# Kernel optimization log

Measured on AMD Instinct MI355X. Metric: run time of the kernel, lower is better.

Reference implementation:

```python
import jax, jax.numpy as jnp
import numpy as np

N = 128000      # total nodes
B = 128         # graphs, 1000 nodes each
L = 4           # max_levels
S_MAX = 1000    # max cluster size (<= PositionalEncoding max_len)
H = 128         # hidden dim (all conv output dims equal)
IN_DIM = 128
OUT_DIM = 1
E = 1024000
TEMP = 0.1


def layer_norm(x, g, b, eps=1e-5):
    mu = jnp.mean(x, axis=-1, keepdims=True)
    v = jnp.mean((x - mu) ** 2, axis=-1, keepdims=True)
    return (x - mu) * jax.lax.rsqrt(v + eps) * g + b


def transformer_conv(x, src, dst, Wq, bq, Wk, bk, Wv, bv, Ws, bs):
    # PyG TransformerConv, heads=1: softmax over in-edges of each dst node
    q = x @ Wq + bq
    k = x @ Wk + bk
    v = x @ Wv + bv
    logits = jnp.sum(q[dst] * k[src], axis=-1) / jnp.sqrt(jnp.float32(q.shape[-1]))
    m = jax.ops.segment_max(logits, dst, num_segments=N)
    e = jnp.exp(logits - m[dst])
    s = jax.ops.segment_sum(e, dst, num_segments=N)
    alpha = e / s[dst]
    agg = jax.ops.segment_sum(alpha[:, None] * v[src], dst, num_segments=N)
    return agg + x @ Ws + bs  # root_weight skip connection


def pos_encoding(S, d):
    pos = jnp.arange(S, dtype=jnp.float32)[:, None]
    div = jnp.exp(jnp.arange(0, d, 2, dtype=jnp.float32) * (-jnp.log(10000.0) / d))
    pe = jnp.zeros((S, d), jnp.float32)
    pe = pe.at[:, 0::2].set(jnp.sin(pos * div))
    pe = pe.at[:, 1::2].set(jnp.cos(pos * div))
    return pe


def gru(xseq, Wih, Whh, bih, bhh):
    # xseq: [G, S, H] -> outputs [G, S, H]; torch GRU gate math
    G = xseq.shape[0]
    def step(h, x_t):
        gi = x_t @ Wih.T + bih
        gh = h @ Whh.T + bhh
        ir, iz, inn = jnp.split(gi, 3, axis=-1)
        hr, hz, hn = jnp.split(gh, 3, axis=-1)
        r = jax.nn.sigmoid(ir + hr)
        z = jax.nn.sigmoid(iz + hz)
        n = jnp.tanh(inn + r * hn)
        h_new = (1.0 - z) * n + z * h
        return h_new, h_new
    h0 = jnp.zeros((G, Whh.shape[1]), xseq.dtype)
    _, outs = jax.lax.scan(step, h0, jnp.swapaxes(xseq, 0, 1))
    return jnp.swapaxes(outs, 0, 1)


def _forward(x, tree_edge_index, call_sequences, batch,
             conv_Wq, conv_bq, conv_Wk, conv_bk, conv_Wv, conv_bv, conv_Ws, conv_bs,
             ln_g, ln_b, centers, proj_W, proj_b,
             gru_Wih, gru_Whh, gru_bih, gru_bhh, seqln_g, seqln_b,
             lin1_W, lin1_b, lin2_W, lin2_b):
    src, dst = tree_edge_index[0], tree_edge_index[1]
    h = x
    for i in range(3):  # conv1/bn1, conv2/bn2, conv4/bn4
        h = transformer_conv(h, src, dst, conv_Wq[i], conv_bq[i], conv_Wk[i],
                             conv_bk[i], conv_Wv[i], conv_bv[i], conv_Ws[i], conv_bs[i])
        h = jax.nn.relu(layer_norm(h, ln_g[i], ln_b[i]))

    # HierarchicalClassifier: cosine-sim soft assignment + center variance loss
    xn = h / jnp.maximum(jnp.linalg.norm(h, axis=-1, keepdims=True), 1e-8)
    cn = centers / jnp.maximum(jnp.linalg.norm(centers, axis=-1, keepdims=True), 1e-8)
    assign = jax.nn.softmax((xn @ cn.T) / TEMP, axis=-1)
    level_ids = jnp.argmax(assign, axis=1).astype(jnp.int32)
    iu0, iu1 = np.triu_indices(L, k=1)
    dvec = jnp.linalg.norm(centers[iu0] - centers[iu1], axis=-1)
    distance = -jnp.var(dvec, ddof=1)  # torch.var is unbiased

    # ragged gather + pad: group nodes by (graph, cluster), sort by call order
    G = B * L
    group = batch * L + level_ids                       # [N]
    order = jnp.argsort(group * N + call_sequences)     # sort by group, then call
    g_sorted = group[order]
    counts = jax.ops.segment_sum(jnp.ones((N,), jnp.int32), group, num_segments=G)
    starts = jnp.cumsum(counts) - counts
    pos = jnp.arange(N, dtype=jnp.int32) - starts[g_sorted]
    seq = jnp.zeros((G, S_MAX, H), h.dtype).at[g_sorted, pos].set(h[order])

    # SequentialRNN: proj -> pos-enc -> GRU -> LayerNorm -> ReLU (mask unused)
    sin = seq @ proj_W + proj_b + pos_encoding(S_MAX, H)[None]
    outs = gru(sin, gru_Wih, gru_Whh, gru_bih, gru_bhh)
    outs = jax.nn.relu(layer_norm(outs, seqln_g, seqln_b))

    # scatter valid positions back; singleton clusters keep raw features
    node_out = jnp.zeros_like(h).at[order].set(outs[g_sorted, pos])
    singleton = (counts[group] == 1)
    gout = jnp.where(singleton[:, None], h, node_out)

    y = jax.nn.gelu(gout @ lin1_W + lin1_b, approximate=False)
    y = jax.nn.sigmoid(y @ lin2_W + lin2_b)
    return y, distance


def setup_inputs():
    key = jax.random.key(0)
    ks = jax.random.split(key, 16)
    p = lambda k, s: jax.random.normal(k, s, jnp.float32) * 0.02
    return {
        "x": jax.random.normal(ks[0], (N, IN_DIM), jnp.float32),
        "tree_edge_index": jax.random.randint(ks[1], (2, E), 0, N, dtype=jnp.int32),
        "call_sequences": jax.random.permutation(ks[2], N).astype(jnp.int32),
        "batch": (jnp.arange(N, dtype=jnp.int32) * B) // N,  # 1000 nodes per graph
        "conv_Wq": p(ks[3], (3, H, H)), "conv_bq": jnp.zeros((3, H), jnp.float32),
        "conv_Wk": p(ks[4], (3, H, H)), "conv_bk": jnp.zeros((3, H), jnp.float32),
        "conv_Wv": p(ks[5], (3, H, H)), "conv_bv": jnp.zeros((3, H), jnp.float32),
        "conv_Ws": p(ks[6], (3, H, H)), "conv_bs": jnp.zeros((3, H), jnp.float32),
        "ln_g": jnp.ones((3, H), jnp.float32), "ln_b": jnp.zeros((3, H), jnp.float32),
        "centers": jax.random.normal(ks[7], (L, H), jnp.float32),
        "proj_W": p(ks[8], (H, H)), "proj_b": jnp.zeros((H,), jnp.float32),
        "gru_Wih": p(ks[9], (3 * H, H)), "gru_Whh": p(ks[10], (3 * H, H)),
        "gru_bih": jnp.zeros((3 * H,), jnp.float32), "gru_bhh": jnp.zeros((3 * H,), jnp.float32),
        "seqln_g": jnp.ones((H,), jnp.float32), "seqln_b": jnp.zeros((H,), jnp.float32),
        "lin1_W": p(ks[11], (H, 8)), "lin1_b": jnp.zeros((8,), jnp.float32),
        "lin2_W": p(ks[12], (8, OUT_DIM)), "lin2_b": jnp.zeros((OUT_DIM,), jnp.float32),
    }


def reference(x, tree_edge_index, call_sequences, batch,
              conv_Wq, conv_bq, conv_Wk, conv_bk, conv_Wv, conv_bv, conv_Ws, conv_bs,
              ln_g, ln_b, centers, proj_W, proj_b,
              gru_Wih, gru_Whh, gru_bih, gru_bhh, seqln_g, seqln_b,
              lin1_W, lin1_b, lin2_W, lin2_b):
    return _forward(x, tree_edge_index, call_sequences, batch,
                    conv_Wq, conv_bq, conv_Wk, conv_bk, conv_Wv, conv_bv, conv_Ws, conv_bs,
                    ln_g, ln_b, centers, proj_W, proj_b,
                    gru_Wih, gru_Whh, gru_bih, gru_bhh, seqln_g, seqln_b,
                    lin1_W, lin1_b, lin2_W, lin2_b)
```

## Files before the change

kernel.cpp:

```cpp
#include <hip/hip_runtime.h>

#define NN 128000
#define EE 1024000
#define HH 128
#define GG 512
#define SMAX 1000
#define NCHUNK 500

typedef unsigned int u32;
typedef unsigned short u16;

constexpr size_t NH     = (size_t)NN*HH;
constexpr size_t F_H    = 0;
constexpr size_t F_A    = NH;
constexpr size_t F_B    = 2*NH;
constexpr size_t F_NODE = F_A + (size_t)NN*192;
constexpr size_t F_QB   = 3*NH;
constexpr size_t F_CN   = F_QB   + NN;
constexpr size_t F_WKT  = F_CN   + 512;
constexpr size_t F_WQK  = F_WKT  + 3*16384;
constexpr size_t F_BQK  = F_WQK  + 3*16384;
constexpr size_t F_WQBK = F_BQK  + 3*128;
constexpr size_t F_QBB  = F_WQBK + 3*128;
constexpr size_t F_CW   = F_QBB  + 8;
constexpr size_t F_PEW  = F_CW   + 128*384;
constexpr size_t F_PEB  = F_PEW  + 1000*384;
constexpr size_t F_END  = F_PEB  + 1000*128;

constexpr size_t I_ROWP = 0;
constexpr size_t I_CUR  = I_ROWP + NN + 8;
constexpr size_t I_COL  = I_CUR  + NN;
constexpr size_t I_GRP  = I_COL  + EE;
constexpr size_t I_INV  = I_GRP  + NN;
constexpr size_t I_POS  = I_INV  + NN;
constexpr size_t I_GN   = I_POS  + NN;
constexpr size_t I_CNT  = I_GN   + (size_t)GG*SMAX;
constexpr size_t I_CH   = I_CNT  + GG;
constexpr size_t I_BS   = I_CH   + (size_t)NCHUNK*GG;
constexpr size_t I_WT   = I_BS   + 512;
constexpr size_t I_END  = I_WT   + 64*384;

constexpr size_t WS_NEEDED = F_END*4 + I_END*4;

__device__ inline float wredf(float v){
  #pragma unroll
  for (int o = 32; o; o >>= 1) v += __shfl_xor(v, o);
  return v;
}
__device__ inline u32 bf16rne(float f){
  u32 u = __float_as_uint(f);
  return (u + 0x7fffu + ((u >> 16) & 1u)) >> 16;
}
__device__ inline float bf2f(u16 u){
  return __uint_as_float(((u32)u) << 16);
}
__device__ inline float frcp(float x){
#if __has_builtin(__builtin_amdgcn_rcpf)
  return __builtin_amdgcn_rcpf(x);
#else
  return 1.f / x;
#endif
}

typedef _Float16 h2_t __attribute__((ext_vector_type(2)));
__device__ inline float dot2f(u32 w, u32 h, float acc){
#if __has_builtin(__builtin_amdgcn_fdot2)
  return __builtin_amdgcn_fdot2(__builtin_bit_cast(h2_t, w),
                                __builtin_bit_cast(h2_t, h), acc, false);
#else
  float r;
  asm("v_dot2_f32_f16 %0, %1, %2, %3" : "=v"(r) : "v"(w), "v"(h), "v"(acc));
  return r;
#endif
}
#define PIN4(v) asm volatile("" : "+v"((v).x), "+v"((v).y), "+v"((v).z), "+v"((v).w))

__global__ void k_sentinel(float* __restrict__ out, int n, float val){
  int i = blockIdx.x * 256 + threadIdx.x;
  if (i < n) out[i] = val;
}

__global__ void k_zero(int* __restrict__ p){
  p[blockIdx.x * 256 + threadIdx.x] = 0;
}
__global__ void k_hist(const int* __restrict__ dst, int* __restrict__ deg){
  int e = blockIdx.x * 256 + threadIdx.x;
  atomicAdd(&deg[dst[e]], 1);
}
__global__ void k_s1(const int* __restrict__ deg, int* __restrict__ bsum){
  __shared__ int red[256];
  int t = threadIdx.x;
  red[t] = deg[blockIdx.x * 256 + t];
  __syncthreads();
  for (int s = 128; s; s >>= 1){ if (t < s) red[t] += red[t + s]; __syncthreads(); }
  if (!t) bsum[blockIdx.x] = red[0];
}
__global__ void k_s2(int* __restrict__ bsum){
  __shared__ int arr[512];
  int t = threadIdx.x;
  int v0 = (t < NCHUNK) ? bsum[t] : 0;
  arr[t] = v0; __syncthreads();
  for (int off = 1; off < 512; off <<= 1){
    int v = (t >= off) ? arr[t - off] : 0;
    __syncthreads();
    arr[t] += v;
    __syncthreads();
  }
  if (t < NCHUNK) bsum[t] = arr[t] - v0;
}
__global__ void k_s3(const int* __restrict__ bsum, int* __restrict__ row_ptr,
                     int* __restrict__ cursor){
  __shared__ int arr[256];
  int t = threadIdx.x;
  int i = blockIdx.x * 256 + t;
  int v0 = cursor[i];
  arr[t] = v0; __syncthreads();
  for (int off = 1; off < 256; off <<= 1){
    int v = (t >= off) ? arr[t - off] : 0;
    __syncthreads();
    arr[t] += v;
    __syncthreads();
  }
  int exc = arr[t] - v0 + bsum[blockIdx.x];
  row_ptr[i] = exc;
  cursor[i]  = exc;
  if (i == 0) row_ptr[NN] = EE;
}
__global__ void k_scatter(const int* __restrict__ src, const int* __restrict__ dst,
                          int* __restrict__ cursor, int* __restrict__ col){
  int e = blockIdx.x * 256 + threadIdx.x;
  int idx = atomicAdd(&cursor[dst[e]], 1);
  col[idx] = src[e];
}

__global__ void k_setup(const float* __restrict__ centers, float* __restrict__ cn,
                        float* __restrict__ dist_out){
  __shared__ float red[128];
  int t = threadIdx.x;
  for (int l = 0; l < 4; ++l){
    float v = centers[l*128 + t];
    red[t] = v * v; __syncthreads();
    for (int s = 64; s; s >>= 1){ if (t < s) red[t] += red[t + s]; __syncthreads(); }
    float nrm = sqrtf(red[0]);
    __syncthreads();
    cn[l*128 + t] = v / fmaxf(nrm, 1e-8f);
  }
  const int iu0[6] = {0,0,0,1,1,2}, iu1[6] = {1,2,3,2,3,3};
  __shared__ float dv[6];
  for (int p = 0; p < 6; ++p){
    float d = centers[iu0[p]*128 + t] - centers[iu1[p]*128 + t];
    red[t] = d * d; __syncthreads();
    for (int s = 64; s; s >>= 1){ if (t < s) red[t] += red[t + s]; __syncthreads(); }
    if (!t) dv[p] = sqrtf(red[0]);
    __syncthreads();
  }
  if (!t){
    float mean = 0.f;
    for (int p = 0; p < 6; ++p) mean += dv[p];
    mean /= 6.f;
    float var = 0.f;
    for (int p = 0; p < 6; ++p){ float d = dv[p] - mean; var += d * d; }
    var /= 5.f;
    dist_out[0] = -var;
  }
}

__global__ void k_pe(const float* __restrict__ projb, float* __restrict__ peb){
  int p = blockIdx.x, t = threadIdx.x;
  float ex  = (float)(t >> 1) * (-2.0f * 9.210340371976184f / 128.0f);
  float ang = (float)p * expf(ex);
  float v = (t & 1) ? cosf(ang) : sinf(ang);
  peb[p*128 + t] = v + projb[t];
}
__global__ void k_pew(const float* __restrict__ peb, const float* __restrict__ Wih,
                      const float* __restrict__ bih, float* __restrict__ pew){
  int p = blockIdx.x;
  int j = blockIdx.y * 128 + threadIdx.x;
  const float* pb = peb + p*128;
  const float* wr = Wih + (size_t)j*128;
  float acc = bih[j];
  #pragma unroll 4
  for (int m = 0; m < 128; ++m) acc += pb[m] * wr[m];
  pew[(size_t)p*384 + j] = acc;
}
__global__ void k_combw(const float* __restrict__ projW, const float* __restrict__ Wih,
                        float* __restrict__ cw){
  int kk = blockIdx.x;
  int j  = blockIdx.y * 128 + threadIdx.x;
  const float* pr = projW + (size_t)kk*128;
  const float* wr = Wih + (size_t)j*128;
  float acc = 0.f;
  #pragma unroll 4
  for (int m = 0; m < 128; ++m) acc += pr[m] * wr[m];
  cw[(size_t)kk*384 + j] = acc;
}
__global__ void k_tr(const float* __restrict__ Wk, float* __restrict__ wkt){
  int kk = blockIdx.x, l = blockIdx.y, c = threadIdx.x;
  wkt[(size_t)l*16384 + kk*128 + c] = Wk[(size_t)l*16384 + c*128 + kk];
}
__global__ void k_mv(const float* __restrict__ M, const float* __restrict__ v,
                     float* __restrict__ out){
  int l = blockIdx.x, i = threadIdx.x;
  const float* row = M + (size_t)l*16384 + (size_t)i*128;
  const float* vv = v + l*128;
  float acc = 0.f;
  #pragma unroll 4
  for (int j = 0; j < 128; ++j) acc += row[j] * vv[j];
  out[l*128 + i] = acc;
}
__global__ void k_bb(const float* __restrict__ bq, const float* __restrict__ bk,
                     float* __restrict__ qbb){
  __shared__ float red[128];
  int l = blockIdx.x, t = threadIdx.x;
  red[t] = bq[l*128 + t] * bk[l*128 + t];
  __syncthreads();
  for (int s = 64; s; s >>= 1){ if (t < s) red[t] += red[t + s]; __syncthreads(); }
  if (!t) qbb[l] = red[0];
}
__global__ void k_packwhh16(const float* __restrict__ Whh, u32* __restrict__ wt){
  int kp = blockIdx.x;
  int j  = blockIdx.y * 128 + threadIdx.x;
  _Float16 a = (_Float16)Whh[(size_t)j*128 + 2*kp];
  _Float16 b = (_Float16)Whh[(size_t)j*128 + 2*kp + 1];
  u32 lo = (u32)__builtin_bit_cast(u16, a);
  u32 hi = (u32)__builtin_bit_cast(u16, b);
  wt[(size_t)j*64 + kp] = (hi << 16) | lo;
}

__global__ __launch_bounds__(256, 2) void k_gemm(
    const float* __restrict__ X, const float* __restrict__ W, int ldw,
    const float* __restrict__ X2, const float* __restrict__ W2,
    const float* __restrict__ bias, const float* __restrict__ pew,
    const int* __restrict__ pos, float* __restrict__ out,
    u16* __restrict__ outb, int ldo){
  __shared__ __align__(16) float Wl[64*132];
  __shared__ __align__(16) float Xl[64*132];
  int tid = threadIdx.x;
  int rb = blockIdx.x * 128;
  int cb = blockIdx.y * 128;
  int rg = tid >> 4;
  int cg = tid & 15;
  int kxor = (cg >> 2) & 3;
  float acc[8][8];
  #pragma unroll
  for (int a = 0; a < 8; ++a)
    #pragma unroll
    for (int b = 0; b < 8; ++b) acc[a][b] = 0.f;
  int nhalf = X2 ? 4 : 2;
  for (int half = 0; half < nhalf; ++half){
    const float* Xs = (half < 2) ? X : X2;
    const float* Ws = (half < 2) ? W : W2;
    int ldws = (half < 2) ? ldw : 128;
    int hk = half & 1;
    __syncthreads();
    #pragma unroll
    for (int it = 0; it < 8; ++it){
      int idx = it*256 + tid;
      int kk = idx >> 5, c4 = idx & 31;
      *(float4*)&Wl[kk*132 + c4*4] =
          *(const float4*)&Ws[(size_t)(hk*64 + kk)*ldws + cb + c4*4];
    }
    #pragma unroll
    for (int it = 0; it < 8; ++it){
      int idx = it*256 + tid;
      int r = idx >> 4, c4 = idx & 15;
      float4 xv = *(const float4*)&Xs[(size_t)(rb + r)*128 + hk*64 + c4*4];
      Xl[(c4*4+0)*132 + r] = xv.x;
      Xl[(c4*4+1)*132 + r] = xv.y;
      Xl[(c4*4+2)*132 + r] = xv.z;
      Xl[(c4*4+3)*132 + r] = xv.w;
    }
    __syncthreads();
    #pragma unroll 2
    for (int kk = 0; kk < 64; ++kk){
      int kx = kk ^ kxor;
      float4 wa = *(const float4*)&Wl[kx*132 + cg*8];
      float4 wb = *(const float4*)&Wl[kx*132 + cg*8 + 4];
      float4 xa = *(const float4*)&Xl[kx*132 + rg*8];
      float4 xb = *(const float4*)&Xl[kx*132 + rg*8 + 4];
      float xs[8] = {xa.x, xa.y, xa.z, xa.w, xb.x, xb.y, xb.z, xb.w};
      float ws[8] = {wa.x, wa.y, wa.z, wa.w, wb.x, wb.y, wb.z, wb.w};
      #pragma unroll
      for (int rr = 0; rr < 8; ++rr)
        #pragma unroll
        for (int j = 0; j < 8; ++j) acc[rr][j] += xs[rr] * ws[j];
    }
  }
  #pragma unroll
  for (int rr = 0; rr < 8; ++rr){
    int r = rb + rg*8 + rr;
    float bv[8];
    if (pos){
      const float* pw = pew + (size_t)pos[r]*384 + cb + cg*8;
      #pragma unroll
      for (int j = 0; j < 8; ++j) bv[j] = pw[j];
    } else if (bias){
      #pragma unroll
      for (int j = 0; j < 8; ++j) bv[j] = bias[cb + cg*8 + j];
    } else {
      #pragma unroll
      for (int j = 0; j < 8; ++j) bv[j] = 0.f;
    }
    if (outb){
      u16 ob[8];
      #pragma unroll
      for (int j = 0; j < 8; ++j) ob[j] = (u16)bf16rne(acc[rr][j] + bv[j]);
      *(uint4*)(outb + (size_t)r*ldo + cb + cg*8) = *(const uint4*)ob;
    } else {
      float ov[8];
      #pragma unroll
      for (int j = 0; j < 8; ++j) ov[j] = acc[rr][j] + bv[j];
      float* op = out + (size_t)r*ldo + cb + cg*8;
      *(float4*)op       = *(const float4*)&ov[0];
      *(float4*)(op + 4) = *(const float4*)&ov[4];
    }
  }
}

__global__ __launch_bounds__(256) void k_rowdot(
    const float* __restrict__ x, const float* __restrict__ w,
    const float* __restrict__ scal, float* __restrict__ qb){
  int d = blockIdx.x * 4 + (threadIdx.x >> 6);
  int lane = threadIdx.x & 63;
  float2 xv = *(const float2*)&x[(size_t)d*128 + 2*lane];
  float2 wv = *(const float2*)&w[2*lane];
  float p = wredf(xv.x * wv.x + xv.y * wv.y);
  if (lane == 0) qb[d] = p + scal[0];
}

__global__ __launch_bounds__(256) void k_edge(
    const float* __restrict__ qt, const float* __restrict__ qb,
    const float* __restrict__ xsrc, const int* __restrict__ row_ptr,
    const int* __restrict__ col, float* __restrict__ xagg){
  int d = blockIdx.x * 8 + (threadIdx.x >> 5);
  int lane = threadIdx.x & 31;
  int e0 = row_ptr[d], e1 = row_ptr[d+1];
  if (e0 == e1){
    *(float4*)&xagg[(size_t)d*128 + lane*4] = make_float4(0.f, 0.f, 0.f, 0.f);
    return;
  }
  float4 qv = *(const float4*)&qt[(size_t)d*128 + lane*4];
  float qbd = qb[d];
  float ssum = 0.f, a0 = 0.f, a1 = 0.f, a2 = 0.f, a3 = 0.f;
  float4 xc = *(const float4*)&xsrc[(size_t)col[e0]*128 + lane*4];
  for (int e = e0; e < e1; ++e){
    float4 xn = xc;
    if (e + 1 < e1)
      xn = *(const float4*)&xsrc[(size_t)col[e+1]*128 + lane*4];
    float p = qv.x*xc.x + qv.y*xc.y + qv.z*xc.z + qv.w*xc.w;
    #pragma unroll
    for (int o = 16; o; o >>= 1) p += __shfl_xor(p, o);
    float el = __expf((p + qbd) * 0.08838834764831845f);
    ssum += el;
    a0 += el * xc.x; a1 += el * xc.y; a2 += el * xc.z; a3 += el * xc.w;
    xc = xn;
  }
  float inv = 1.f / ssum;
  *(float4*)&xagg[(size_t)d*128 + lane*4] =
      make_float4(a0*inv, a1*inv, a2*inv, a3*inv);
}

__global__ __launch_bounds__(256) void k_lnrelu(
    const float* __restrict__ in, const float* __restrict__ g,
    const float* __restrict__ b, const float* __restrict__ bvv,
    const int* __restrict__ rowp, float* __restrict__ outp){
  int node = blockIdx.x * 4 + (threadIdx.x >> 6);
  int lane = threadIdx.x & 63;
  float x0 = in[(size_t)node*128 + 2*lane], x1 = in[(size_t)node*128 + 2*lane + 1];
  if (bvv && rowp[node+1] > rowp[node]){
    x0 += bvv[2*lane];
    x1 += bvv[2*lane + 1];
  }
  float s = wredf(x0 + x1);
  float qq = wredf(x0*x0 + x1*x1);
  float mu = s * 0.0078125f;
  float var = qq * 0.0078125f - mu*mu;
  float rstd = rsqrtf(var + 1e-5f);
  float y0 = (x0 - mu)*rstd*g[2*lane]   + b[2*lane];
  float y1 = (x1 - mu)*rstd*g[2*lane+1] + b[2*lane+1];
  outp[(size_t)node*128 + 2*lane]     = fmaxf(y0, 0.f);
  outp[(size_t)node*128 + 2*lane + 1] = fmaxf(y1, 0.f);
}

__global__ __launch_bounds__(256) void k_lnrelu_cls(
    const float* __restrict__ in, const float* __restrict__ g,
    const float* __restrict__ b, const float* __restrict__ bvv,
    const int* __restrict__ rowp, float* __restrict__ outp,
    const float* __restrict__ cn, const int* __restrict__ batch,
    const int* __restrict__ callsq, int* __restrict__ grp, int* __restrict__ inv){
  int node = blockIdx.x * 4 + (threadIdx.x >> 6);
  int lane = threadIdx.x & 63;
  float x0 = in[(size_t)node*128 + 2*lane], x1 = in[(size_t)node*128 + 2*lane + 1];
  if (rowp[node+1] > rowp[node]){
    x0 += bvv[2*lane];
    x1 += bvv[2*lane + 1];
  }
  float s = wredf(x0 + x1);
  float qq = wredf(x0*x0 + x1*x1);
  float mu = s * 0.0078125f;
  float var = qq * 0.0078125f - mu*mu;
  float rstd = rsqrtf(var + 1e-5f);
  float y0 = fmaxf((x0 - mu)*rstd*g[2*lane]   + b[2*lane],   0.f);
  float y1 = fmaxf((x1 - mu)*rstd*g[2*lane+1] + b[2*lane+1], 0.f);
  outp[(size_t)node*128 + 2*lane]     = y0;
  outp[(size_t)node*128 + 2*lane + 1] = y1;
  float p0 = y0*cn[      2*lane] + y1*cn[      2*lane+1];
  float p1 = y0*cn[128 + 2*lane] + y1*cn[128 + 2*lane+1];
  float p2 = y0*cn[256 + 2*lane] + y1*cn[256 + 2*lane+1];
  float p3 = y0*cn[384 + 2*lane] + y1*cn[384 + 2*lane+1];
  p0 = wredf(p0); p1 = wredf(p1); p2 = wredf(p2); p3 = wredf(p3);
  if (lane == 0){
    float best = p0; int bi = 0;
    if (p1 > best){ best = p1; bi = 1; }
    if (p2 > best){ best = p2; bi = 2; }
    if (p3 > best){ best = p3; bi = 3; }
    grp[node] = batch[node]*4 + bi;
    inv[callsq[node]] = node;
  }
}

__global__ __launch_bounds__(256) void k_g1(const int* __restrict__ inv,
                                            const int* __restrict__ grp,
                                            int* __restrict__ ch){
  __shared__ int hist[GG];
  int c = blockIdx.x, t = threadIdx.x;
  hist[t] = 0; hist[t + 256] = 0;
  __syncthreads();
  int g = grp[inv[c*256 + t]];
  atomicAdd(&hist[g], 1);
  __syncthreads();
  ch[c*GG + t] = hist[t];
  ch[c*GG + 256 + t] = hist[256 + t];
}
__global__ void k_g2(int* __restrict__ ch, int* __restrict__ cnt){
  __shared__ int arr[512];
  int g = blockIdx.x, t = threadIdx.x;
  int v0 = (t < NCHUNK) ? ch[(size_t)t*GG + g] : 0;
  arr[t] = v0; __syncthreads();
  for (int off = 1; off < 512; off <<= 1){
    int v = (t >= off) ? arr[t - off] : 0;
    __syncthreads();
    arr[t] += v;
    __syncthreads();
  }
  if (t < NCHUNK) ch[(size_t)t*GG + g] = arr[t] - v0;
  if (t == 511) cnt[g] = arr[511];
}
__global__ __launch_bounds__(256) void k_g3(
    const int* __restrict__ inv, const int* __restrict__ grp,
    const int* __restrict__ ch, int* __restrict__ pos, int* __restrict__ gn){
  __shared__ int hist[GG];
  int c = blockIdx.x, t = threadIdx.x;
  hist[t] = 0; hist[t + 256] = 0;
  __syncthreads();
  int node = inv[c*256 + t];
  int g = grp[node];
  int lane = t & 63, w = t >> 6;
  int before = 0, total = 0;
  for (int j = 0; j < 64; ++j){
    int gj = __shfl(g, j);
    if (gj == g){ total++; if (j < lane) before++; }
  }
  int base = 0;
  for (int wv = 0; wv < 4; ++wv){
    if (w == wv){
      base = hist[g];
      if (before == total - 1) hist[g] = base + total;
    }
    __syncthreads();
  }
  int p = ch[c*GG + g] + base + before;
  pos[node] = p;
  gn[(size_t)g*SMAX + p] = node;
}

__global__ __launch_bounds__(256)
__attribute__((amdgpu_waves_per_eu(2, 2)))
void k_gru(
    const u16* __restrict__ gi, const u32* __restrict__ wt,
    const float* __restrict__ bhh, const int* __restrict__ gn,
    const int* __restrict__ cnt, u16* __restrict__ node_out){
  __shared__ __align__(16) u16 hb16[2][128];
  int t = threadIdx.x;
  int j = t >> 1;
  int kh = t & 1;
  int g = blockIdx.x;
  int my = cnt[g];
  if (my <= 1) return;
  uint4 wr_[8], wz_[8], wn_[8];
  {
    const uint4* wt4 = (const uint4*)wt;
    size_t b0 = (size_t)(0*128 + j)*16 + kh*8;
    size_t b1 = (size_t)(1*128 + j)*16 + kh*8;
    size_t b2 = (size_t)(2*128 + j)*16 + kh*8;
    #pragma unroll
    for (int s = 0; s < 8; ++s){
      wr_[s] = wt4[b0 + s];
      wz_[s] = wt4[b1 + s];
      wn_[s] = wt4[b2 + s];
    }
    #pragma unroll
    for (int s = 0; s < 8; ++s){
      PIN4(wr_[s]); PIN4(wz_[s]); PIN4(wn_[s]);
    }
  }
  if (t < 128) hb16[0][t] = 0;
  float br = bhh[j], bz = bhh[128 + j], bn = bhh[256 + j];
  const int* gnr = gn + (size_t)g*SMAX;
  float hprev = 0.f;
  int nA = gnr[0];
  int nB = gnr[min(1, my - 1)];
  int nC = gnr[min(2, my - 1)];
  const u16* gA = gi + (size_t)nA*384;
  const u16* gB = gi + (size_t)nB*384;
  const u16* gC = gi + (size_t)nC*384;
  float axr = bf2f(gA[j]), axz = bf2f(gA[128 + j]), axn = bf2f(gA[256 + j]);
  float bxr = bf2f(gB[j]), bxz = bf2f(gB[128 + j]), bxn = bf2f(gB[256 + j]);
  float cxr = bf2f(gC[j]), cxz = bf2f(gC[128 + j]), cxn = bf2f(gC[256 + j]);
  __syncthreads();
  for (int p = 0; p < my; ++p){
    int cur = p & 1, nxt = cur ^ 1;
    float xr = axr, xz = axz, xn = axn;
    int node = nA;
    axr = bxr; axz = bxz; axn = bxn; nA = nB;
    bxr = cxr; bxz = cxz; bxn = cxn; nB = nC;
    nC = gnr[min(p + 3, my - 1)];
    const u16* gN = gi + (size_t)nC*384;
    cxr = bf2f(gN[j]); cxz = bf2f(gN[128 + j]); cxn = bf2f(gN[256 + j]);
    const uint4* HB = (const uint4*)&hb16[cur][0];
    uint4 hh[8];
    #pragma unroll
    for (int s = 0; s < 8; ++s) hh[s] = HB[kh*8 + s];
    __builtin_amdgcn_s_setprio(1);
    float ar = 0.f, az = 0.f, an = 0.f;
    #pragma unroll
    for (int s = 0; s < 8; ++s){
      ar = dot2f(wr_[s].x, hh[s].x, ar); az = dot2f(wz_[s].x, hh[s].x, az); an = dot2f(wn_[s].x, hh[s].x, an);
      ar = dot2f(wr_[s].y, hh[s].y, ar); az = dot2f(wz_[s].y, hh[s].y, az); an = dot2f(wn_[s].y, hh[s].y, an);
      ar = dot2f(wr_[s].z, hh[s].z, ar); az = dot2f(wz_[s].z, hh[s].z, az); an = dot2f(wn_[s].z, hh[s].z, an);
      ar = dot2f(wr_[s].w, hh[s].w, ar); az = dot2f(wz_[s].w, hh[s].w, az); an = dot2f(wn_[s].w, hh[s].w, an);
    }
    ar += __shfl_xor(ar, 1); az += __shfl_xor(az, 1); an += __shfl_xor(an, 1);
    ar += br; az += bz; an += bn;
    float er = __expf(-(xr + ar));
    float r  = frcp(1.f + er);
    float ez = __expf(-(xz + az));
    float z  = frcp(1.f + ez);
    float y  = xn + r * an;
    float e2 = __expf(-2.f * y);
    float n  = (1.f - e2) * frcp(1.f + e2);
    float hnew = n + z * (hprev - n);
    __builtin_amdgcn_s_setprio(0);
    hprev = hnew;
    if (!kh){
      _Float16 hf = (_Float16)hnew;
      hb16[nxt][j] = __builtin_bit_cast(u16, hf);
      node_out[(size_t)node*128 + j] = (u16)bf16rne(hnew);
    }
    __syncthreads();
  }
}

__global__ __launch_bounds__(256) void k_head(
    const float* __restrict__ h, const u16* __restrict__ node_out,
    const int* __restrict__ grp, const int* __restrict__ cnt,
    const float* __restrict__ sqg, const float* __restrict__ sqb,
    const float* __restrict__ l1W, const float* __restrict__ l1b,
    const float* __restrict__ l2W, const float* __restrict__ l2b,
    float* __restrict__ out){
  int node = blockIdx.x * 4 + (threadIdx.x >> 6);
  int lane = threadIdx.x & 63;
  bool single = (cnt[grp[node]] == 1);
  float x0, x1;
  if (single){
    x0 = h[(size_t)node*128 + 2*lane];
    x1 = h[(size_t)node*128 + 2*lane + 1];
  } else {
    float r0 = bf2f(node_out[(size_t)node*128 + 2*lane]);
    float r1 = bf2f(node_out[(size_t)node*128 + 2*lane + 1]);
    float s = wredf(r0 + r1);
    float qq = wredf(r0*r0 + r1*r1);
    float mu = s * 0.0078125f;
    float var = qq * 0.0078125f - mu*mu;
    float rstd = rsqrtf(var + 1e-5f);
    x0 = fmaxf((r0 - mu)*rstd*sqg[2*lane]   + sqb[2*lane],   0.f);
    x1 = fmaxf((r1 - mu)*rstd*sqg[2*lane+1] + sqb[2*lane+1], 0.f);
  }
  float acc[8];
  #pragma unroll
  for (int j = 0; j < 8; ++j)
    acc[j] = x0 * l1W[(2*lane)*8 + j] + x1 * l1W[(2*lane + 1)*8 + j];
  #pragma unroll
  for (int o = 32; o; o >>= 1)
    #pragma unroll
    for (int j = 0; j < 8; ++j) acc[j] += __shfl_xor(acc[j], o);
  if (lane == 0){
    float zz = l2b[0];
    #pragma unroll
    for (int j = 0; j < 8; ++j){
      float xx = acc[j] + l1b[j];
      float ge = 0.5f * xx * (1.f + erff(xx * 0.7071067811865476f));
      zz += ge * l2W[j];
    }
    out[node] = 1.f / (1.f + expf(-zz));
  }
}

extern "C" void kernel_launch(void* const* d_in, const int* in_sizes, int n_in,
                              void* d_out, int out_size, void* d_ws, size_t ws_size,
                              hipStream_t stream){
  float* out = (float*)d_out;

  if (ws_size < WS_NEEDED){
    float code = -(float)(ws_size >> 20);
    k_sentinel<<<(out_size + 255)/256, 256, 0, stream>>>(out, out_size, code);
    return;
  }

  const float* x       = (const float*)d_in[0];
  const int*   tei     = (const int*)d_in[1];
  const int*   callsq  = (const int*)d_in[2];
  const int*   batch   = (const int*)d_in[3];
  const float* Wq      = (const float*)d_in[4];
  const float* bq      = (const float*)d_in[5];
  const float* Wk      = (const float*)d_in[6];
  const float* bk      = (const float*)d_in[7];
  const float* Wv      = (const float*)d_in[8];
  const float* bv      = (const float*)d_in[9];
  const float* Wsk     = (const float*)d_in[10];
  const float* bsk     = (const float*)d_in[11];
  const float* lng     = (const float*)d_in[12];
  const float* lnb     = (const float*)d_in[13];
  const float* centers = (const float*)d_in[14];
  const float* projW   = (const float*)d_in[15];
  const float* projb   = (const float*)d_in[16];
  const float* Wih     = (const float*)d_in[17];
  const float* Whh     = (const float*)d_in[18];
  const float* bih     = (const float*)d_in[19];
  const float* bhh     = (const float*)d_in[20];
  const float* sqg     = (const float*)d_in[21];
  const float* sqb     = (const float*)d_in[22];
  const float* l1W     = (const float*)d_in[23];
  const float* l1b     = (const float*)d_in[24];
  const float* l2W     = (const float*)d_in[25];
  const float* l2b     = (const float*)d_in[26];

  float* wf = (float*)d_ws;
  float* f_h    = wf + F_H;
  float* f_a    = wf + F_A;
  float* f_b    = wf + F_B;
  float* f_qb   = wf + F_QB;
  float* f_cn   = wf + F_CN;
  float* f_wkt  = wf + F_WKT;
  float* f_wqk  = wf + F_WQK;
  float* f_bqk  = wf + F_BQK;
  float* f_wqbk = wf + F_WQBK;
  float* f_qbb  = wf + F_QBB;
  float* f_cw   = wf + F_CW;
  float* f_pew  = wf + F_PEW;
  float* f_peb  = wf + F_PEB;
  u16*   gi_bf  = (u16*)(wf + F_A);
  u16*   no_bf  = (u16*)(wf + F_NODE);
  int* wi = (int*)(wf + F_END);
  int* i_rowp = wi + I_ROWP;
  int* i_cur  = wi + I_CUR;
  int* i_col  = wi + I_COL;
  int* i_grp  = wi + I_GRP;
  int* i_inv  = wi + I_INV;
  int* i_pos  = wi + I_POS;
  int* i_gn   = wi + I_GN;
  int* i_cnt  = wi + I_CNT;
  int* i_ch   = wi + I_CH;
  int* i_bs   = wi + I_BS;
  u32* i_wt   = (u32*)(wi + I_WT);

  const int* esrc = tei;
  const int* edst = tei + EE;

  k_zero<<<NN/256, 256, 0, stream>>>(i_cur);
  k_hist<<<EE/256, 256, 0, stream>>>(edst, i_cur);
  k_s1<<<NCHUNK, 256, 0, stream>>>(i_cur, i_bs);
  k_s2<<<1, 512, 0, stream>>>(i_bs);
  k_s3<<<NCHUNK, 256, 0, stream>>>(i_bs, i_rowp, i_cur);
  k_scatter<<<EE/256, 256, 0, stream>>>(esrc, edst, i_cur, i_col);

  k_setup<<<1, 128, 0, stream>>>(centers, f_cn, out + NN);
  k_pe<<<1000, 128, 0, stream>>>(projb, f_peb);
  k_pew<<<dim3(1000, 3), 128, 0, stream>>>(f_peb, Wih, bih, f_pew);
  k_tr<<<dim3(128, 3), 128, 0, stream>>>(Wk, f_wkt);
  for (int i = 0; i < 3; ++i)
    k_gemm<<<dim3(1, 1), 256, 0, stream>>>(Wq + (size_t)i*16384, f_wkt + (size_t)i*16384,
        128, nullptr, nullptr, nullptr, nullptr, nullptr, f_wqk + (size_t)i*16384,
        nullptr, 128);
  k_mv<<<3, 128, 0, stream>>>(Wq, bk, f_wqbk);
  k_mv<<<3, 128, 0, stream>>>(Wk, bq, f_bqk);
  k_bb<<<3, 128, 0, stream>>>(bq, bk, f_qbb);
  k_combw<<<dim3(128, 3), 128, 0, stream>>>(projW, Wih, f_cw);
  k_packwhh16<<<dim3(64, 3), 128, 0, stream>>>(Whh, i_wt);

  for (int i = 0; i < 3; ++i){
    const float* xin = i ? f_h : x;
    size_t wo = (size_t)i * 128 * 128, bo = (size_t)i * 128;
    k_gemm<<<dim3(NN/128, 1), 256, 0, stream>>>(xin, f_wqk + (size_t)i*16384, 128,
        nullptr, nullptr, f_bqk + bo, nullptr, nullptr, f_b, nullptr, 128);
    k_rowdot<<<NN/4, 256, 0, stream>>>(xin, f_wqbk + bo, f_qbb + i, f_qb);
    k_edge<<<NN/8, 256, 0, stream>>>(f_b, f_qb, xin, i_rowp, i_col, f_a);
    k_gemm<<<dim3(NN/128, 1), 256, 0, stream>>>(f_a, Wv + wo, 128, xin, Wsk + wo,
        bsk + bo, nullptr, nullptr, f_b, nullptr, 128);
    if (i < 2)
      k_lnrelu<<<NN/4, 256, 0, stream>>>(f_b, lng + bo, lnb + bo, bv + bo, i_rowp, f_h);
    else
      k_lnrelu_cls<<<NN/4, 256, 0, stream>>>(f_b, lng + bo, lnb + bo, bv + bo, i_rowp,
          f_h, f_cn, batch, callsq, i_grp, i_inv);
  }

  k_g1<<<NCHUNK, 256, 0, stream>>>(i_inv, i_grp, i_ch);
  k_g2<<<GG, 512, 0, stream>>>(i_ch, i_cnt);
  k_g3<<<NCHUNK, 256, 0, stream>>>(i_inv, i_grp, i_ch, i_pos, i_gn);

  k_gemm<<<dim3(NN/128, 3), 256, 0, stream>>>(f_h, f_cw, 384, nullptr, nullptr,
      nullptr, f_pew, i_pos, nullptr, gi_bf, 384);

  k_gru<<<GG, 256, 0, stream>>>(gi_bf, i_wt, bhh, i_gn, i_cnt, no_bf);

  k_head<<<NN/4, 256, 0, stream>>>(f_h, no_bf, i_grp, i_cnt, sqg, sqb,
                                   l1W, l1b, l2W, l2b, out);
}
```

Measured before the change: 2.258 ms.

## Drop softmax-invariant query bias term and fuse LayerNorm+ReLU into GEMM epilogue

Removes the per-destination bias dot-product kernel and its precompute (k_rowdot, k_bb, one k_mv). That term is constant within each destination's softmax, so it cancels. For the first two conv layers, LayerNorm and ReLU are folded into the epilogue of the value/skip GEMM. Row statistics are reduced across the 16 column-group lanes, which avoids a separate read/write pass over the node features. The edge aggregation loop is also unrolled by two with independent accumulators in place of the software prefetch. This trades extra epilogue registers in the GEMM, which may affect occupancy, for fewer kernel launches and less memory traffic.

```diff
diff --git a/kernel.cpp b/kernel.cpp
--- a/kernel.cpp
+++ b/kernel.cpp
@@ -15,14 +15,11 @@
 constexpr size_t F_A    = NH;
 constexpr size_t F_B    = 2*NH;
 constexpr size_t F_NODE = F_A + (size_t)NN*192;
-constexpr size_t F_QB   = 3*NH;
-constexpr size_t F_CN   = F_QB   + NN;
+constexpr size_t F_CN   = 3*NH;
 constexpr size_t F_WKT  = F_CN   + 512;
 constexpr size_t F_WQK  = F_WKT  + 3*16384;
 constexpr size_t F_BQK  = F_WQK  + 3*16384;
-constexpr size_t F_WQBK = F_BQK  + 3*128;
-constexpr size_t F_QBB  = F_WQBK + 3*128;
-constexpr size_t F_CW   = F_QBB  + 8;
+constexpr size_t F_CW   = F_BQK  + 3*128;
 constexpr size_t F_PEW  = F_CW   + 128*384;
 constexpr size_t F_PEB  = F_PEW  + 1000*384;
 constexpr size_t F_END  = F_PEB  + 1000*128;
@@ -208,15 +205,6 @@
   for (int j = 0; j < 128; ++j) acc += row[j] * vv[j];
   out[l*128 + i] = acc;
 }
-__global__ void k_bb(const float* __restrict__ bq, const float* __restrict__ bk,
-                     float* __restrict__ qbb){
-  __shared__ float red[128];
-  int l = blockIdx.x, t = threadIdx.x;
-  red[t] = bq[l*128 + t] * bk[l*128 + t];
-  __syncthreads();
-  for (int s = 64; s; s >>= 1){ if (t < s) red[t] += red[t + s]; __syncthreads(); }
-  if (!t) qbb[l] = red[0];
-}
 __global__ void k_packwhh16(const float* __restrict__ Whh, u32* __restrict__ wt){
   int kp = blockIdx.x;
   int j  = blockIdx.y * 128 + threadIdx.x;
@@ -232,7 +220,9 @@
     const float* __restrict__ X2, const float* __restrict__ W2,
     const float* __restrict__ bias, const float* __restrict__ pew,
     const int* __restrict__ pos, float* __restrict__ out,
-    u16* __restrict__ outb, int ldo){
+    u16* __restrict__ outb, int ldo,
+    const float* __restrict__ lng, const float* __restrict__ lnb,
+    const float* __restrict__ bvv, const int* __restrict__ rowp){
   __shared__ __align__(16) float Wl[64*132];
   __shared__ __align__(16) float Xl[64*132];
   int tid = threadIdx.x;
@@ -286,6 +276,39 @@
         for (int j = 0; j < 8; ++j) acc[rr][j] += xs[rr] * ws[j];
     }
   }
+  if (lng){
+    float gv[8], bl[8], bb[8], vv[8];
+    #pragma unroll
+    for (int j = 0; j < 8; ++j){
+      int c = cg*8 + j;
+      gv[j] = lng[c]; bl[j] = lnb[c]; bb[j] = bias[c]; vv[j] = bvv[c];
+    }
+    #pragma unroll
+    for (int rr = 0; rr < 8; ++rr){
+      int r = rb + rg*8 + rr;
+      bool deg = rowp[r+1] > rowp[r];
+      float rs = 0.f, rq = 0.f;
+      #pragma unroll
+      for (int j = 0; j < 8; ++j){
+        float v = acc[rr][j] + bb[j] + (deg ? vv[j] : 0.f);
+        acc[rr][j] = v;
+        rs += v; rq += v*v;
+      }
+      #pragma unroll
+      for (int o = 8; o; o >>= 1){ rs += __shfl_xor(rs, o); rq += __shfl_xor(rq, o); }
+      float mu = rs * 0.0078125f;
+      float var = rq * 0.0078125f - mu*mu;
+      float rstd = rsqrtf(var + 1e-5f);
+      float ov[8];
+      #pragma unroll
+      for (int j = 0; j < 8; ++j)
+        ov[j] = fmaxf((acc[rr][j] - mu)*rstd*gv[j] + bl[j], 0.f);
+      float* op = out + (size_t)r*128 + cg*8;
+      *(float4*)op       = *(const float4*)&ov[0];
+      *(float4*)(op + 4) = *(const float4*)&ov[4];
+    }
+    return;
+  }
   #pragma unroll
   for (int rr = 0; rr < 8; ++rr){
     int r = rb + rg*8 + rr;
@@ -317,21 +340,10 @@
   }
 }
 
-__global__ __launch_bounds__(256) void k_rowdot(
-    const float* __restrict__ x, const float* __restrict__ w,
-    const float* __restrict__ scal, float* __restrict__ qb){
-  int d = blockIdx.x * 4 + (threadIdx.x >> 6);
-  int lane = threadIdx.x & 63;
-  float2 xv = *(const float2*)&x[(size_t)d*128 + 2*lane];
-  float2 wv = *(const float2*)&w[2*lane];
-  float p = wredf(xv.x * wv.x + xv.y * wv.y);
-  if (lane == 0) qb[d] = p + scal[0];
-}
-
 __global__ __launch_bounds__(256) void k_edge(
-    const float* __restrict__ qt, const float* __restrict__ qb,
-    const float* __restrict__ xsrc, const int* __restrict__ row_ptr,
-    const int* __restrict__ col, float* __restrict__ xagg){
+    const float* __restrict__ qt, const float* __restrict__ xsrc,
+    const int* __restrict__ row_ptr, const int* __restrict__ col,
+    float* __restrict__ xagg){
   int d = blockIdx.x * 8 + (threadIdx.x >> 5);
   int lane = threadIdx.x & 31;
   int e0 = row_ptr[d], e1 = row_ptr[d+1];
@@ -339,47 +351,36 @@
     *(float4*)&xagg[(size_t)d*128 + lane*4] = make_float4(0.f, 0.f, 0.f, 0.f);
     return;
   }
+  const float S = 0.08838834764831845f;
   float4 qv = *(const float4*)&qt[(size_t)d*128 + lane*4];
-  float qbd = qb[d];
-  float ssum = 0.f, a0 = 0.f, a1 = 0.f, a2 = 0.f, a3 = 0.f;
-  float4 xc = *(const float4*)&xsrc[(size_t)col[e0]*128 + lane*4];
-  for (int e = e0; e < e1; ++e){
-    float4 xn = xc;
-    if (e + 1 < e1)
-      xn = *(const float4*)&xsrc[(size_t)col[e+1]*128 + lane*4];
-    float p = qv.x*xc.x + qv.y*xc.y + qv.z*xc.z + qv.w*xc.w;
-    #pragma unroll
-    for (int o = 16; o; o >>= 1) p += __shfl_xor(p, o);
-    float el = __expf((p + qbd) * 0.08838834764831845f);
-    ssum += el;
-    a0 += el * xc.x; a1 += el * xc.y; a2 += el * xc.z; a3 += el * xc.w;
-    xc = xn;
-  }
-  float inv = 1.f / ssum;
+  float ss0 = 0.f, ss1 = 0.f;
+  float4 A0 = make_float4(0.f,0.f,0.f,0.f), A1 = make_float4(0.f,0.f,0.f,0.f);
+  int e = e0;
+  for (; e + 1 < e1; e += 2){
+    float4 x0 = *(const float4*)&xsrc[(size_t)col[e]  *128 + lane*4];
+    float4 x1 = *(const float4*)&xsrc[(size_t)col[e+1]*128 + lane*4];
+    float p0 = qv.x*x0.x + qv.y*x0.y + qv.z*x0.z + qv.w*x0.w;
+    float p1 = qv.x*x1.x + qv.y*x1.y + qv.z*x1.z + qv.w*x1.w;
+    #pragma unroll
+    for (int o = 16; o; o >>= 1){ p0 += __shfl_xor(p0, o); p1 += __shfl_xor(p1, o); }
+    float el0 = __expf(p0 * S);
+    float el1 = __expf(p1 * S);
+    ss0 += el0; ss1 += el1;
+    A0.x += el0*x0.x; A0.y += el0*x0.y; A0.z += el0*x0.z; A0.w += el0*x0.w;
+    A1.x += el1*x1.x; A1.y += el1*x1.y; A1.z += el1*x1.z; A1.w += el1*x1.w;
+  }
+  if (e < e1){
+    float4 x0 = *(const float4*)&xsrc[(size_t)col[e]*128 + lane*4];
+    float p0 = qv.x*x0.x + qv.y*x0.y + qv.z*x0.z + qv.w*x0.w;
+    #pragma unroll
+    for (int o = 16; o; o >>= 1) p0 += __shfl_xor(p0, o);
+    float el0 = __expf(p0 * S);
+    ss0 += el0;
+    A0.x += el0*x0.x; A0.y += el0*x0.y; A0.z += el0*x0.z; A0.w += el0*x0.w;
+  }
+  float inv = 1.f / (ss0 + ss1);
   *(float4*)&xagg[(size_t)d*128 + lane*4] =
-      make_float4(a0*inv, a1*inv, a2*inv, a3*inv);
-}
-
-__global__ __launch_bounds__(256) void k_lnrelu(
-    const float* __restrict__ in, const float* __restrict__ g,
-    const float* __restrict__ b, const float* __restrict__ bvv,
-    const int* __restrict__ rowp, float* __restrict__ outp){
-  int node = blockIdx.x * 4 + (threadIdx.x >> 6);
-  int lane = threadIdx.x & 63;
-  float x0 = in[(size_t)node*128 + 2*lane], x1 = in[(size_t)node*128 + 2*lane + 1];
-  if (bvv && rowp[node+1] > rowp[node]){
-    x0 += bvv[2*lane];
-    x1 += bvv[2*lane + 1];
-  }
-  float s = wredf(x0 + x1);
-  float qq = wredf(x0*x0 + x1*x1);
-  float mu = s * 0.0078125f;
-  float var = qq * 0.0078125f - mu*mu;
-  float rstd = rsqrtf(var + 1e-5f);
-  float y0 = (x0 - mu)*rstd*g[2*lane]   + b[2*lane];
-  float y1 = (x1 - mu)*rstd*g[2*lane+1] + b[2*lane+1];
-  outp[(size_t)node*128 + 2*lane]     = fmaxf(y0, 0.f);
-  outp[(size_t)node*128 + 2*lane + 1] = fmaxf(y1, 0.f);
+      make_float4((A0.x+A1.x)*inv, (A0.y+A1.y)*inv, (A0.z+A1.z)*inv, (A0.w+A1.w)*inv);
 }
 
 __global__ __launch_bounds__(256) void k_lnrelu_cls(
@@ -649,13 +650,10 @@
   float* f_h    = wf + F_H;
   float* f_a    = wf + F_A;
   float* f_b    = wf + F_B;
-  float* f_qb   = wf + F_QB;
   float* f_cn   = wf + F_CN;
   float* f_wkt  = wf + F_WKT;
   float* f_wqk  = wf + F_WQK;
   float* f_bqk  = wf + F_BQK;
-  float* f_wqbk = wf + F_WQBK;
-  float* f_qbb  = wf + F_QBB;
   float* f_cw   = wf + F_CW;
   float* f_pew  = wf + F_PEW;
   float* f_peb  = wf + F_PEB;
@@ -691,10 +689,8 @@
   for (int i = 0; i < 3; ++i)
     k_gemm<<<dim3(1, 1), 256, 0, stream>>>(Wq + (size_t)i*16384, f_wkt + (size_t)i*16384,
         128, nullptr, nullptr, nullptr, nullptr, nullptr, f_wqk + (size_t)i*16384,
-        nullptr, 128);
-  k_mv<<<3, 128, 0, stream>>>(Wq, bk, f_wqbk);
+        nullptr, 128, nullptr, nullptr, nullptr, nullptr);
   k_mv<<<3, 128, 0, stream>>>(Wk, bq, f_bqk);
-  k_bb<<<3, 128, 0, stream>>>(bq, bk, f_qbb);
   k_combw<<<dim3(128, 3), 128, 0, stream>>>(projW, Wih, f_cw);
   k_packwhh16<<<dim3(64, 3), 128, 0, stream>>>(Whh, i_wt);
 
@@ -702,16 +698,20 @@
     const float* xin = i ? f_h : x;
     size_t wo = (size_t)i * 128 * 128, bo = (size_t)i * 128;
     k_gemm<<<dim3(NN/128, 1), 256, 0, stream>>>(xin, f_wqk + (size_t)i*16384, 128,
-        nullptr, nullptr, f_bqk + bo, nullptr, nullptr, f_b, nullptr, 128);
-    k_rowdot<<<NN/4, 256, 0, stream>>>(xin, f_wqbk + bo, f_qbb + i, f_qb);
-    k_edge<<<NN/8, 256, 0, stream>>>(f_b, f_qb, xin, i_rowp, i_col, f_a);
-    k_gemm<<<dim3(NN/128, 1), 256, 0, stream>>>(f_a, Wv + wo, 128, xin, Wsk + wo,
-        bsk + bo, nullptr, nullptr, f_b, nullptr, 128);
-    if (i < 2)
-      k_lnrelu<<<NN/4, 256, 0, stream>>>(f_b, lng + bo, lnb + bo, bv + bo, i_rowp, f_h);
-    else
+        nullptr, nullptr, f_bqk + bo, nullptr, nullptr, f_b, nullptr, 128,
+        nullptr, nullptr, nullptr, nullptr);
+    k_edge<<<NN/8, 256, 0, stream>>>(f_b, xin, i_rowp, i_col, f_a);
+    if (i < 2){
+      k_gemm<<<dim3(NN/128, 1), 256, 0, stream>>>(f_a, Wv + wo, 128, xin, Wsk + wo,
+          bsk + bo, nullptr, nullptr, f_h, nullptr, 128,
+          lng + bo, lnb + bo, bv + bo, i_rowp);
+    } else {
+      k_gemm<<<dim3(NN/128, 1), 256, 0, stream>>>(f_a, Wv + wo, 128, xin, Wsk + wo,
+          bsk + bo, nullptr, nullptr, f_b, nullptr, 128,
+          nullptr, nullptr, nullptr, nullptr);
       k_lnrelu_cls<<<NN/4, 256, 0, stream>>>(f_b, lng + bo, lnb + bo, bv + bo, i_rowp,
           f_h, f_cn, batch, callsq, i_grp, i_inv);
+    }
   }
 
   k_g1<<<NCHUNK, 256, 0, stream>>>(i_inv, i_grp, i_ch);
@@ -719,7 +719,7 @@
   k_g3<<<NCHUNK, 256, 0, stream>>>(i_inv, i_grp, i_ch, i_pos, i_gn);
 
   k_gemm<<<dim3(NN/128, 3), 256, 0, stream>>>(f_h, f_cw, 384, nullptr, nullptr,
-      nullptr, f_pew, i_pos, nullptr, gi_bf, 384);
+      nullptr, f_pew, i_pos, nullptr, gi_bf, 384, nullptr, nullptr, nullptr, nullptr);
 
   k_gru<<<GG, 256, 0, stream>>>(gi_bf, i_wt, bhh, i_gn, i_cnt, no_bf);
 
```

Result: faster. 2.118 ms (-6.2%).
